# Optimization experiments

Hardware: AMD Instinct MI355X
Metric: run time of the kernel (lower is better)

Reference implementation:

```python
import jax, jax.numpy as jnp
import numpy as np

N_ENT = 50000
N_REL = 500
N_EDGE = 800000
H_DIM = 96
BN_EPS = 1e-5


def setup_inputs() -> dict:
    key = jax.random.key(0)
    k1, k2, k3, k4, k5 = jax.random.split(key, 5)
    return {
        "ent_emb": jax.random.normal(k1, (N_ENT, H_DIM), dtype=jnp.float32),
        "rel_emb": jax.random.normal(k2, (N_REL, H_DIM), dtype=jnp.float32),
        "neigh_w": jax.random.normal(k3, (H_DIM, H_DIM), dtype=jnp.float32) * (1.0 / np.sqrt(H_DIM)),
        "bn_gamma": jnp.ones((H_DIM,), dtype=jnp.float32),
        "bn_beta": jnp.zeros((H_DIM,), dtype=jnp.float32),
        "rel_id": jax.random.randint(k4, (N_EDGE,), 0, N_REL, dtype=jnp.int64),
        "dst": jax.random.randint(k5, (N_EDGE,), 0, N_ENT, dtype=jnp.int64),
    }


def reference(ent_emb, rel_emb, neigh_w, bn_gamma, bn_beta, rel_id, dst):
    n_nodes = ent_emb.shape[0]
    # per-edge gather: edge feature = relation embedding  [E, D]
    e = rel_emb[rel_id]
    # e_dot_v: dot of edge feature with destination node embedding  [E]
    score = jnp.sum(e * ent_emb[dst], axis=-1)
    # edge softmax over incoming edges of each destination node
    seg_max = jax.ops.segment_max(score, dst, num_segments=n_nodes)  # [N]
    w = jnp.exp(score - seg_max[dst])                                # [E]
    seg_sum = jax.ops.segment_sum(w, dst, num_segments=n_nodes)      # [N]
    alpha = w / seg_sum[dst]                                         # [E]
    # weighted scatter-sum aggregation into destination nodes  [N, D]
    neigh = jax.ops.segment_sum(e * alpha[:, None], dst, num_segments=n_nodes)
    # linear
    out = neigh @ neigh_w
    # BatchNorm1d (training mode: batch stats over nodes, biased var)
    mu = jnp.mean(out, axis=0)
    var = jnp.mean((out - mu) ** 2, axis=0)
    out = (out - mu) * jax.lax.rsqrt(var + BN_EPS) * bn_gamma + bn_beta
    return jnp.tanh(out)
```

## Files before the change

### kernel.cpp

```cpp
#include <hip/hip_runtime.h>
#include <math.h>

#define N_ENT   50000
#define N_REL   500
#define N_EDGE  800000
#define H       96
#define BN_EPS  1e-5f
#define DEG_CAP 64

#define RELW_BLOCKS ((N_REL * H + 255) / 256)
#define ZERO_N      (N_ENT + 2 * H)
#define ZERO_BLOCKS ((ZERO_N + 255) / 256)

__global__ __launch_bounds__(256) void k_init(
        const float* __restrict__ rel, const float* __restrict__ W,
        float* __restrict__ relW, unsigned* __restrict__ zbase) {
    if (blockIdx.x < RELW_BLOCKS) {
        __shared__ float Ws[H * H];
        for (int i = threadIdx.x; i < H * H; i += 256) Ws[i] = W[i];
        __syncthreads();
        int t = blockIdx.x * 256 + threadIdx.x;
        if (t >= N_REL * H) return;
        int r = t / H;
        int c = t - r * H;
        const float4* rr = (const float4*)(rel + (size_t)r * H);
        float acc = 0.0f;
#pragma unroll
        for (int i = 0; i < H / 4; ++i) {
            float4 a = rr[i];
            acc += a.x * Ws[(4 * i + 0) * H + c];
            acc += a.y * Ws[(4 * i + 1) * H + c];
            acc += a.z * Ws[(4 * i + 2) * H + c];
            acc += a.w * Ws[(4 * i + 3) * H + c];
        }
        relW[t] = acc;
    } else {
        int i = (blockIdx.x - RELW_BLOCKS) * 256 + threadIdx.x;
        if (i < ZERO_N) zbase[i] = 0u;
    }
}

__global__ __launch_bounds__(256) void k_bucket(
        const int* __restrict__ dst, const int* __restrict__ rel_id,
        int* __restrict__ cursor, unsigned short* __restrict__ pay) {
    int i = blockIdx.x * 256 + threadIdx.x;
    if (i >= N_EDGE / 4) return;
    int4 d = ((const int4*)dst)[i];
    int4 r = ((const int4*)rel_id)[i];
    int p;
    p = atomicAdd(cursor + d.x, 1); if (p < DEG_CAP) pay[d.x * DEG_CAP + p] = (unsigned short)r.x;
    p = atomicAdd(cursor + d.y, 1); if (p < DEG_CAP) pay[d.y * DEG_CAP + p] = (unsigned short)r.y;
    p = atomicAdd(cursor + d.z, 1); if (p < DEG_CAP) pay[d.z * DEG_CAP + p] = (unsigned short)r.z;
    p = atomicAdd(cursor + d.w, 1); if (p < DEG_CAP) pay[d.w * DEG_CAP + p] = (unsigned short)r.w;
}

__global__ __launch_bounds__(256) void k_node(
        const float* __restrict__ ent, const float* __restrict__ rel,
        const unsigned short* __restrict__ pay, const int* __restrict__ cursor,
        const float* __restrict__ relW, float* __restrict__ out) {
    __shared__ float sh_w[4][DEG_CAP];
    __shared__ int   sh_r[4][DEG_CAP];
    int wv   = threadIdx.x >> 6;
    int lane = threadIdx.x & 63;
    int n = blockIdx.x * 4 + wv;
    if (n >= N_ENT) return;
    int cnt = min(cursor[n], DEG_CAP);

    int q  = lane & 3;
    int jj = lane >> 2;
    const float4* er = (const float4*)(ent + (size_t)n * H) + q * 6;
    float4 e0 = er[0], e1 = er[1], e2 = er[2], e3 = er[3], e4 = er[4], e5 = er[5];
    int npass = (cnt + 15) >> 4;
    for (int p = 0; p < npass; ++p) {
        int j = (p << 4) + jj;
        bool valid = (j < cnt);
        int rid = valid ? (int)pay[n * DEG_CAP + j] : 0;
        float part = 0.0f;
        if (valid) {
            const float4* rr = (const float4*)(rel + (size_t)rid * H) + q * 6;
            float4 b;
            b = rr[0]; part += e0.x*b.x + e0.y*b.y + e0.z*b.z + e0.w*b.w;
            b = rr[1]; part += e1.x*b.x + e1.y*b.y + e1.z*b.z + e1.w*b.w;
            b = rr[2]; part += e2.x*b.x + e2.y*b.y + e2.z*b.z + e2.w*b.w;
            b = rr[3]; part += e3.x*b.x + e3.y*b.y + e3.z*b.z + e3.w*b.w;
            b = rr[4]; part += e4.x*b.x + e4.y*b.y + e4.z*b.z + e4.w*b.w;
            b = rr[5]; part += e5.x*b.x + e5.y*b.y + e5.z*b.z + e5.w*b.w;
        }
        part += __shfl_xor(part, 1);
        part += __shfl_xor(part, 2);
        if (valid && q == 0) { sh_w[wv][j] = part; sh_r[wv][j] = rid; }
    }

    float sc = (lane < cnt) ? sh_w[wv][lane] : -INFINITY;
    float m = sc;
#pragma unroll
    for (int off = 1; off < 64; off <<= 1)
        m = fmaxf(m, __shfl_xor(m, off));
    float w = (lane < cnt) ? __expf(sc - m) : 0.0f;
    float s = w;
#pragma unroll
    for (int off = 1; off < 64; off <<= 1)
        s += __shfl_xor(s, off);
    if (lane < cnt) sh_w[wv][lane] = w;
    float inv = (cnt > 0) ? 1.0f / s : 0.0f;

    int pl = (lane < H / 4) ? lane : 0;
    float4 acc0 = make_float4(0.f, 0.f, 0.f, 0.f);
    float4 acc1 = make_float4(0.f, 0.f, 0.f, 0.f);
    int k = 0;
    for (; k + 2 <= cnt; k += 2) {
        float a0 = sh_w[wv][k],     a1 = sh_w[wv][k + 1];
        int   r0 = sh_r[wv][k],     r1 = sh_r[wv][k + 1];
        float4 f0 = ((const float4*)(relW + (size_t)r0 * H))[pl];
        float4 f1 = ((const float4*)(relW + (size_t)r1 * H))[pl];
        acc0.x += a0 * f0.x; acc0.y += a0 * f0.y;
        acc0.z += a0 * f0.z; acc0.w += a0 * f0.w;
        acc1.x += a1 * f1.x; acc1.y += a1 * f1.y;
        acc1.z += a1 * f1.z; acc1.w += a1 * f1.w;
    }
    if (k < cnt) {
        float a0 = sh_w[wv][k];
        int   r0 = sh_r[wv][k];
        float4 f0 = ((const float4*)(relW + (size_t)r0 * H))[pl];
        acc0.x += a0 * f0.x; acc0.y += a0 * f0.y;
        acc0.z += a0 * f0.z; acc0.w += a0 * f0.w;
    }
    if (lane < H / 4) {
        float4 o = make_float4((acc0.x + acc1.x) * inv, (acc0.y + acc1.y) * inv,
                               (acc0.z + acc1.z) * inv, (acc0.w + acc1.w) * inv);
        ((float4*)(out + (size_t)n * H))[lane] = o;
    }
}

__global__ __launch_bounds__(256) void k_bnstats(
        const float* __restrict__ out, float* __restrict__ bn_sum,
        float* __restrict__ bn_sumsq) {
    __shared__ float sh_s[4][H], sh_q[4][H];
    int wave = threadIdx.x >> 6;
    int lane = threadIdx.x & 63;
    float4 s = make_float4(0.f, 0.f, 0.f, 0.f);
    float4 ss = make_float4(0.f, 0.f, 0.f, 0.f);
    if (lane < H / 4) {
        for (int n = blockIdx.x * 4 + wave; n < N_ENT; n += gridDim.x * 4) {
            float4 v = ((const float4*)(out + (size_t)n * H))[lane];
            s.x += v.x; s.y += v.y; s.z += v.z; s.w += v.w;
            ss.x += v.x * v.x; ss.y += v.y * v.y;
            ss.z += v.z * v.z; ss.w += v.w * v.w;
        }
        ((float4*)sh_s[wave])[lane] = s;
        ((float4*)sh_q[wave])[lane] = ss;
    }
    __syncthreads();
    int d = threadIdx.x;
    if (d < H) {
        float ts = sh_s[0][d] + sh_s[1][d] + sh_s[2][d] + sh_s[3][d];
        float tq = sh_q[0][d] + sh_q[1][d] + sh_q[2][d] + sh_q[3][d];
        atomicAdd(bn_sum + d, ts);
        atomicAdd(bn_sumsq + d, tq);
    }
}

__device__ __forceinline__ float fast_tanh(float x) {
    return 1.0f - 2.0f / (__expf(2.0f * x) + 1.0f);
}

__global__ __launch_bounds__(256) void k_bnapply(
        float* __restrict__ out, const float* __restrict__ bn_sum,
        const float* __restrict__ bn_sumsq, const float* __restrict__ gamma,
        const float* __restrict__ beta) {
    int t = blockIdx.x * 256 + threadIdx.x;
    if (t >= N_ENT * H / 4) return;
    int c4 = t % (H / 4);
    const float inv_n = 1.0f / (float)N_ENT;
    float4 v = ((const float4*)out)[t];
    float4 sm = ((const float4*)bn_sum)[c4];
    float4 sq = ((const float4*)bn_sumsq)[c4];
    float4 g  = ((const float4*)gamma)[c4];
    float4 b  = ((const float4*)beta)[c4];
    float mu0 = sm.x * inv_n, mu1 = sm.y * inv_n, mu2 = sm.z * inv_n, mu3 = sm.w * inv_n;
    float r0 = rsqrtf(sq.x * inv_n - mu0 * mu0 + BN_EPS);
    float r1 = rsqrtf(sq.y * inv_n - mu1 * mu1 + BN_EPS);
    float r2 = rsqrtf(sq.z * inv_n - mu2 * mu2 + BN_EPS);
    float r3 = rsqrtf(sq.w * inv_n - mu3 * mu3 + BN_EPS);
    float4 o;
    o.x = fast_tanh((v.x - mu0) * r0 * g.x + b.x);
    o.y = fast_tanh((v.y - mu1) * r1 * g.y + b.y);
    o.z = fast_tanh((v.z - mu2) * r2 * g.z + b.z);
    o.w = fast_tanh((v.w - mu3) * r3 * g.w + b.w);
    ((float4*)out)[t] = o;
}

extern "C" void kernel_launch(void* const* d_in, const int* in_sizes, int n_in,
                              void* d_out, int out_size, void* d_ws, size_t ws_size,
                              hipStream_t stream) {
    const float* ent   = (const float*)d_in[0];
    const float* rel   = (const float*)d_in[1];
    const float* W     = (const float*)d_in[2];
    const float* gamma = (const float*)d_in[3];
    const float* beta  = (const float*)d_in[4];
    const int* rel_id  = (const int*)d_in[5];
    const int* dst     = (const int*)d_in[6];
    float* out = (float*)d_out;

    float* ws       = (float*)d_ws;
    int*   cursor   = (int*)ws;
    float* bn_sum   = ws + N_ENT;
    float* bn_sumsq = bn_sum + H;
    float* relW     = bn_sumsq + H;
    unsigned short* pay = (unsigned short*)(relW + N_REL * H);

    k_init<<<RELW_BLOCKS + ZERO_BLOCKS, 256, 0, stream>>>(
        rel, W, relW, (unsigned*)cursor);
    k_bucket<<<(N_EDGE / 4 + 255) / 256, 256, 0, stream>>>(dst, rel_id, cursor, pay);
    k_node<<<(N_ENT + 3) / 4, 256, 0, stream>>>(ent, rel, pay, cursor, relW, out);
    k_bnstats<<<784, 256, 0, stream>>>(out, bn_sum, bn_sumsq);
    k_bnapply<<<(N_ENT * H / 4 + 255) / 256, 256, 0, stream>>>(
        out, bn_sum, bn_sumsq, gamma, beta);
}
```

Before: 215.7 us.

## Use one edge per thread in bucketing and split aggregation across all lanes

```diff
diff --git a/kernel.cpp b/kernel.cpp
--- a/kernel.cpp
+++ b/kernel.cpp
@@ -43,15 +43,12 @@
 __global__ __launch_bounds__(256) void k_bucket(
         const int* __restrict__ dst, const int* __restrict__ rel_id,
         int* __restrict__ cursor, unsigned short* __restrict__ pay) {
-    int i = blockIdx.x * 256 + threadIdx.x;
-    if (i >= N_EDGE / 4) return;
-    int4 d = ((const int4*)dst)[i];
-    int4 r = ((const int4*)rel_id)[i];
-    int p;
-    p = atomicAdd(cursor + d.x, 1); if (p < DEG_CAP) pay[d.x * DEG_CAP + p] = (unsigned short)r.x;
-    p = atomicAdd(cursor + d.y, 1); if (p < DEG_CAP) pay[d.y * DEG_CAP + p] = (unsigned short)r.y;
-    p = atomicAdd(cursor + d.z, 1); if (p < DEG_CAP) pay[d.z * DEG_CAP + p] = (unsigned short)r.z;
-    p = atomicAdd(cursor + d.w, 1); if (p < DEG_CAP) pay[d.w * DEG_CAP + p] = (unsigned short)r.w;
+    int e = blockIdx.x * 256 + threadIdx.x;
+    if (e >= N_EDGE) return;
+    int d = dst[e];
+    int r = rel_id[e];
+    int p = atomicAdd(cursor + d, 1);
+    if (p < DEG_CAP) pay[d * DEG_CAP + p] = (unsigned short)r;
 }
 
 __global__ __launch_bounds__(256) void k_node(
@@ -66,69 +63,74 @@
     if (n >= N_ENT) return;
     int cnt = min(cursor[n], DEG_CAP);
 
-    int q  = lane & 3;
-    int jj = lane >> 2;
-    const float4* er = (const float4*)(ent + (size_t)n * H) + q * 6;
-    float4 e0 = er[0], e1 = er[1], e2 = er[2], e3 = er[3], e4 = er[4], e5 = er[5];
-    int npass = (cnt + 15) >> 4;
-    for (int p = 0; p < npass; ++p) {
-        int j = (p << 4) + jj;
-        bool valid = (j < cnt);
-        int rid = valid ? (int)pay[n * DEG_CAP + j] : 0;
-        float part = 0.0f;
-        if (valid) {
-            const float4* rr = (const float4*)(rel + (size_t)rid * H) + q * 6;
-            float4 b;
-            b = rr[0]; part += e0.x*b.x + e0.y*b.y + e0.z*b.z + e0.w*b.w;
-            b = rr[1]; part += e1.x*b.x + e1.y*b.y + e1.z*b.z + e1.w*b.w;
-            b = rr[2]; part += e2.x*b.x + e2.y*b.y + e2.z*b.z + e2.w*b.w;
-            b = rr[3]; part += e3.x*b.x + e3.y*b.y + e3.z*b.z + e3.w*b.w;
-            b = rr[4]; part += e4.x*b.x + e4.y*b.y + e4.z*b.z + e4.w*b.w;
-            b = rr[5]; part += e5.x*b.x + e5.y*b.y + e5.z*b.z + e5.w*b.w;
+    {
+        int q  = lane & 3;
+        int jj = lane >> 2;
+        const float4* er = (const float4*)(ent + (size_t)n * H) + q * 6;
+        float4 e0 = er[0], e1 = er[1], e2 = er[2], e3 = er[3], e4 = er[4], e5 = er[5];
+        int npass = (cnt + 15) >> 4;
+        for (int p = 0; p < npass; ++p) {
+            int j = (p << 4) + jj;
+            bool valid = (j < cnt);
+            int rid = valid ? (int)pay[n * DEG_CAP + j] : 0;
+            float part = 0.0f;
+            if (valid) {
+                const float4* rr = (const float4*)(rel + (size_t)rid * H) + q * 6;
+                float4 b;
+                b = rr[0]; part += e0.x*b.x + e0.y*b.y + e0.z*b.z + e0.w*b.w;
+                b = rr[1]; part += e1.x*b.x + e1.y*b.y + e1.z*b.z + e1.w*b.w;
+                b = rr[2]; part += e2.x*b.x + e2.y*b.y + e2.z*b.z + e2.w*b.w;
+                b = rr[3]; part += e3.x*b.x + e3.y*b.y + e3.z*b.z + e3.w*b.w;
+                b = rr[4]; part += e4.x*b.x + e4.y*b.y + e4.z*b.z + e4.w*b.w;
+                b = rr[5]; part += e5.x*b.x + e5.y*b.y + e5.z*b.z + e5.w*b.w;
+            }
+            part += __shfl_xor(part, 1);
+            part += __shfl_xor(part, 2);
+            if (valid && q == 0) { sh_w[wv][j] = part; sh_r[wv][j] = rid; }
         }
-        part += __shfl_xor(part, 1);
-        part += __shfl_xor(part, 2);
-        if (valid && q == 0) { sh_w[wv][j] = part; sh_r[wv][j] = rid; }
-    }
-
-    float sc = (lane < cnt) ? sh_w[wv][lane] : -INFINITY;
-    float m = sc;
-#pragma unroll
-    for (int off = 1; off < 64; off <<= 1)
-        m = fmaxf(m, __shfl_xor(m, off));
-    float w = (lane < cnt) ? __expf(sc - m) : 0.0f;
-    float s = w;
-#pragma unroll
-    for (int off = 1; off < 64; off <<= 1)
-        s += __shfl_xor(s, off);
-    if (lane < cnt) sh_w[wv][lane] = w;
-    float inv = (cnt > 0) ? 1.0f / s : 0.0f;
-
-    int pl = (lane < H / 4) ? lane : 0;
-    float4 acc0 = make_float4(0.f, 0.f, 0.f, 0.f);
-    float4 acc1 = make_float4(0.f, 0.f, 0.f, 0.f);
-    int k = 0;
-    for (; k + 2 <= cnt; k += 2) {
-        float a0 = sh_w[wv][k],     a1 = sh_w[wv][k + 1];
-        int   r0 = sh_r[wv][k],     r1 = sh_r[wv][k + 1];
-        float4 f0 = ((const float4*)(relW + (size_t)r0 * H))[pl];
-        float4 f1 = ((const float4*)(relW + (size_t)r1 * H))[pl];
-        acc0.x += a0 * f0.x; acc0.y += a0 * f0.y;
-        acc0.z += a0 * f0.z; acc0.w += a0 * f0.w;
-        acc1.x += a1 * f1.x; acc1.y += a1 * f1.y;
-        acc1.z += a1 * f1.z; acc1.w += a1 * f1.w;
-    }
-    if (k < cnt) {
-        float a0 = sh_w[wv][k];
-        int   r0 = sh_r[wv][k];
-        float4 f0 = ((const float4*)(relW + (size_t)r0 * H))[pl];
-        acc0.x += a0 * f0.x; acc0.y += a0 * f0.y;
-        acc0.z += a0 * f0.z; acc0.w += a0 * f0.w;
-    }
-    if (lane < H / 4) {
-        float4 o = make_float4((acc0.x + acc1.x) * inv, (acc0.y + acc1.y) * inv,
-                               (acc0.z + acc1.z) * inv, (acc0.w + acc1.w) * inv);
-        ((float4*)(out + (size_t)n * H))[lane] = o;
+    }
+
+    {
+        float sc = (lane < cnt) ? sh_w[wv][lane] : -INFINITY;
+        float m = sc;
+#pragma unroll
+        for (int off = 1; off < 64; off <<= 1)
+            m = fmaxf(m, __shfl_xor(m, off));
+        float w = (lane < cnt) ? __expf(sc - m) : 0.0f;
+        float s = w;
+#pragma unroll
+        for (int off = 1; off < 64; off <<= 1)
+            s += __shfl_xor(s, off);
+        float inv = (cnt > 0) ? 1.0f / s : 0.0f;
+        if (lane < cnt) sh_w[wv][lane] = w * inv;
+    }
+
+    int g  = lane & 7;
+    int es = lane >> 3;
+    float4 a0 = make_float4(0.f, 0.f, 0.f, 0.f);
+    float4 a1 = make_float4(0.f, 0.f, 0.f, 0.f);
+    float4 a2 = make_float4(0.f, 0.f, 0.f, 0.f);
+    for (int k = es; k < cnt; k += 8) {
+        float w  = sh_w[wv][k];
+        int rid  = sh_r[wv][k];
+        const float4* p = (const float4*)(relW + (size_t)rid * H + g * 12);
+        float4 f0 = p[0], f1 = p[1], f2 = p[2];
+        a0.x += w * f0.x; a0.y += w * f0.y; a0.z += w * f0.z; a0.w += w * f0.w;
+        a1.x += w * f1.x; a1.y += w * f1.y; a1.z += w * f1.z; a1.w += w * f1.w;
+        a2.x += w * f2.x; a2.y += w * f2.y; a2.z += w * f2.z; a2.w += w * f2.w;
+    }
+#pragma unroll
+    for (int off = 8; off < 64; off <<= 1) {
+        a0.x += __shfl_xor(a0.x, off); a0.y += __shfl_xor(a0.y, off);
+        a0.z += __shfl_xor(a0.z, off); a0.w += __shfl_xor(a0.w, off);
+        a1.x += __shfl_xor(a1.x, off); a1.y += __shfl_xor(a1.y, off);
+        a1.z += __shfl_xor(a1.z, off); a1.w += __shfl_xor(a1.w, off);
+        a2.x += __shfl_xor(a2.x, off); a2.y += __shfl_xor(a2.y, off);
+        a2.z += __shfl_xor(a2.z, off); a2.w += __shfl_xor(a2.w, off);
+    }
+    if (es == 0) {
+        float4* op = (float4*)(out + (size_t)n * H + g * 12);
+        op[0] = a0; op[1] = a1; op[2] = a2;
     }
 }
 
@@ -211,7 +213,7 @@
 
     k_init<<<RELW_BLOCKS + ZERO_BLOCKS, 256, 0, stream>>>(
         rel, W, relW, (unsigned*)cursor);
-    k_bucket<<<(N_EDGE / 4 + 255) / 256, 256, 0, stream>>>(dst, rel_id, cursor, pay);
+    k_bucket<<<(N_EDGE + 255) / 256, 256, 0, stream>>>(dst, rel_id, cursor, pay);
     k_node<<<(N_ENT + 3) / 4, 256, 0, stream>>>(ent, rel, pay, cursor, relW, out);
     k_bnstats<<<784, 256, 0, stream>>>(out, bn_sum, bn_sumsq);
     k_bnapply<<<(N_ENT * H / 4 + 255) / 256, 256, 0, stream>>>(
```

Result: faster. 205.7 us (-4.6%).
